# Kernel tuning notes

Measured on AMD Instinct MI355X. Metric: run time of the kernel, lower is better.

The kernel has to match this reference:

```python
import jax, jax.numpy as jnp
import numpy as np

GRID_SIZE = 3
LN_EPS = 1e-5
BASIS_EPS = 1e-6


def setup_inputs() -> dict:
    key = jax.random.key(0)
    ks = jax.random.split(key, 5)
    B, S, D_IN, D_OUT, SE_H = 8, 1024, 1024, 1024, 32
    x = jax.random.normal(ks[0], (B, S, D_IN), dtype=jnp.float32)
    base_weight = jax.random.normal(ks[1], (D_OUT, D_IN), dtype=jnp.float32) * 0.01
    spline_weight = jax.random.normal(ks[2], (D_OUT, D_IN, GRID_SIZE), dtype=jnp.float32) * 0.005
    ln_w = jnp.ones((D_OUT,), dtype=jnp.float32)
    ln_b = jnp.zeros((D_OUT,), dtype=jnp.float32)
    se_w1 = jax.random.normal(ks[3], (SE_H, D_OUT), dtype=jnp.float32) * 0.03
    se_b1 = jnp.zeros((SE_H,), dtype=jnp.float32)
    se_w2 = jax.random.normal(ks[4], (D_OUT, SE_H), dtype=jnp.float32) * 0.03
    se_b2 = jnp.zeros((D_OUT,), dtype=jnp.float32)
    return {"x": x, "base_weight": base_weight, "spline_weight": spline_weight,
            "ln_w": ln_w, "ln_b": ln_b, "se_w1": se_w1, "se_b1": se_b1,
            "se_w2": se_w2, "se_b2": se_b2}


def _kan_layer(x2d, base_weight, spline_weight, ln_w, ln_b, se_w1, se_b1, se_w2, se_b2):
    # x2d: [N, D_in]
    base = x2d @ base_weight.T                                   # [N, D_out]
    grid = jnp.linspace(-1.0, 1.0, GRID_SIZE).astype(x2d.dtype)  # [G]
    dist = jnp.abs(x2d[..., None] - grid)                        # [N, D_in, G]
    basis = jnp.where(dist < 1.0, (1.0 - dist) ** 2, 0.0)
    basis = basis / (basis.sum(axis=-1, keepdims=True) + BASIS_EPS)
    spline = jnp.einsum('nig,oig->no', basis, spline_weight)     # [N, D_out]
    out = base + spline
    # LayerNorm (dropout is identity at inference)
    mu = out.mean(axis=-1, keepdims=True)
    var = ((out - mu) ** 2).mean(axis=-1, keepdims=True)
    out = (out - mu) * jax.lax.rsqrt(var + LN_EPS) * ln_w + ln_b
    # SE gating (2D branch: applied per flattened token)
    h = jnp.maximum(out @ se_w1.T + se_b1, 0.0)
    se = jax.nn.sigmoid(h @ se_w2.T + se_b2)
    return out * se


def reference(x, base_weight, spline_weight, ln_w, ln_b, se_w1, se_b1, se_w2, se_b2):
    B, S, D = x.shape
    out = _kan_layer(x.reshape(-1, D), base_weight, spline_weight,
                     ln_w, ln_b, se_w1, se_b1, se_w2, se_b2)
    return out.reshape(B, S, -1)
```

## Files before the change

### kernel.cpp

```cpp
#include <hip/hip_runtime.h>
#include <hip/hip_bf16.h>
#include <math.h>

typedef __attribute__((ext_vector_type(8))) __bf16 bf16x8;
typedef __attribute__((ext_vector_type(4))) float f32x4;

#define NTOK 8192
#define DIN 1024
#define DOUT 1024
#define KAUG 4096
#define SEH 32

#define BK 64
#define NKT (KAUG / BK)

static __device__ __forceinline__ unsigned short f2bf(float f) {
  union { float f; unsigned u; } v; v.f = f;
  unsigned r = (v.u + 0x7FFFu + ((v.u >> 16) & 1u)) >> 16;
  return (unsigned short)r;
}

__global__ __launch_bounds__(256) void prep(const float* __restrict__ x,
                                            const float* __restrict__ bw,
                                            const float* __restrict__ sw,
                                            const float* __restrict__ w1,
                                            const float* __restrict__ w2,
                                            ushort* __restrict__ Aaug,
                                            ushort* __restrict__ Waug,
                                            ushort* __restrict__ w1b,
                                            ushort* __restrict__ w2b) {
  const int b = blockIdx.x;
  if (b < 32768) {
    const int id = b * 256 + threadIdx.x;
    const float v = x[id];
    const float d0 = fabsf(v + 1.f), d1 = fabsf(v), d2 = fabsf(v - 1.f);
    float b0 = (d0 < 1.f) ? (1.f - d0) * (1.f - d0) : 0.f;
    float b1 = (d1 < 1.f) ? (1.f - d1) * (1.f - d1) : 0.f;
    float b2 = (d2 < 1.f) ? (1.f - d2) * (1.f - d2) : 0.f;
    const float inv = 1.f / (b0 + b1 + b2 + 1e-6f);
    ushort4 o;
    o.x = f2bf(v);
    o.y = f2bf(b0 * inv);
    o.z = f2bf(b1 * inv);
    o.w = f2bf(b2 * inv);
    ((ushort4*)Aaug)[id] = o;
  } else if (b < 32768 + 4096) {
    const int id = (b - 32768) * 256 + threadIdx.x;
    ushort4 o;
    o.x = f2bf(bw[id]);
    o.y = f2bf(sw[id * 3 + 0]);
    o.z = f2bf(sw[id * 3 + 1]);
    o.w = f2bf(sw[id * 3 + 2]);
    ((ushort4*)Waug)[id] = o;
  } else {
    const int id = (b - 32768 - 4096) * 256 + threadIdx.x;
    if (id < SEH * DOUT) w1b[id] = f2bf(w1[id]);
    else w2b[id - SEH * DOUT] = f2bf(w2[id - SEH * DOUT]);
  }
}

#define WAITVM(N) asm volatile("s_waitcnt vmcnt(" #N ")" ::: "memory")

__global__ __launch_bounds__(256, 2) void gemm_ns(const ushort* __restrict__ A,
                                                  const ushort* __restrict__ B,
                                                  float* __restrict__ C) {
  __shared__ ushort As[2][128 * BK];
  __shared__ ushort Bs[2][128 * BK];
  const int tid = threadIdx.x;
  const int wid = tid >> 6, lane = tid & 63;
  const int l16 = lane & 15, lk = lane >> 4;
  const int wm = wid >> 1, wn = wid & 1;

  const int g = (blockIdx.x & 7) * 64 + (blockIdx.x >> 3);
  const int bm = g >> 3;
  const int bn = g & 7;

  const ushort* Ab = A + (size_t)bm * 128 * KAUG;
  const ushort* Bb = B + (size_t)bn * 128 * KAUG;

  const int lrow = lane >> 3;
  const int lcb = (lane & 7) ^ lrow;

  const int aBase = (wm * 64 + l16) * 64;
  const int bBase = (wn * 64 + l16) * 64;
  const int sw0 = ((l16 & 4) << 3) + ((lk ^ (l16 & 3)) << 3);
  const int sw1 = sw0 ^ 32;

  f32x4 acc[4][4] = {};

#define STAGE_A(kt, buf, r)                                                     \
  __builtin_amdgcn_global_load_lds(                                             \
      (const __attribute__((address_space(1))) void*)(Ab +                      \
          (size_t)((r) * 32 + wid * 8 + lrow) * KAUG + (kt) * BK + lcb * 8),    \
      (__attribute__((address_space(3))) void*)(&As[buf][((r) * 256 + wid * 64) * 8]), \
      16, 0, 0)
#define STAGE_B(kt, buf, r)                                                     \
  __builtin_amdgcn_global_load_lds(                                             \
      (const __attribute__((address_space(1))) void*)(Bb +                      \
          (size_t)((r) * 32 + wid * 8 + lrow) * KAUG + (kt) * BK + lcb * 8),    \
      (__attribute__((address_space(3))) void*)(&Bs[buf][((r) * 256 + wid * 64) * 8]), \
      16, 0, 0)
#define STAGE_ALL(kt, buf)                                                      \
  do {                                                                          \
    STAGE_A(kt, buf, 0); STAGE_A(kt, buf, 1); STAGE_A(kt, buf, 2); STAGE_A(kt, buf, 3); \
    STAGE_B(kt, buf, 0); STAGE_B(kt, buf, 1); STAGE_B(kt, buf, 2); STAGE_B(kt, buf, 3); \
  } while (0)

#define TILE(kt, CB, NB)                                                        \
  do {                                                                          \
    if ((kt) < NKT - 1) {                                                       \
      STAGE_ALL((kt) + 1, NB);                                                  \
      WAITVM(8);                                                                \
    } else {                                                                    \
      WAITVM(0);                                                                \
    }                                                                           \
    __builtin_amdgcn_s_barrier();                                               \
    bf16x8 af0[4], bf0[4], af1[4], bf1[4];                                      \
    _Pragma("unroll")                                                           \
    for (int m = 0; m < 4; ++m) af0[m] = *(const bf16x8*)&As[CB][aBase + m * 1024 + sw0]; \
    _Pragma("unroll")                                                           \
    for (int n = 0; n < 4; ++n) bf0[n] = *(const bf16x8*)&Bs[CB][bBase + n * 1024 + sw0]; \
    __builtin_amdgcn_s_setprio(1);                                              \
    _Pragma("unroll")                                                           \
    for (int m = 0; m < 4; ++m)                                                 \
      _Pragma("unroll")                                                         \
      for (int n = 0; n < 4; ++n)                                               \
        acc[m][n] = __builtin_amdgcn_mfma_f32_16x16x32_bf16(                    \
            af0[m], bf0[n], acc[m][n], 0, 0, 0);                                \
    __builtin_amdgcn_s_setprio(0);                                              \
    _Pragma("unroll")                                                           \
    for (int m = 0; m < 4; ++m) af1[m] = *(const bf16x8*)&As[CB][aBase + m * 1024 + sw1]; \
    _Pragma("unroll")                                                           \
    for (int n = 0; n < 4; ++n) bf1[n] = *(const bf16x8*)&Bs[CB][bBase + n * 1024 + sw1]; \
    __builtin_amdgcn_s_setprio(1);                                              \
    _Pragma("unroll")                                                           \
    for (int m = 0; m < 4; ++m)                                                 \
      _Pragma("unroll")                                                         \
      for (int n = 0; n < 4; ++n)                                               \
        acc[m][n] = __builtin_amdgcn_mfma_f32_16x16x32_bf16(                    \
            af1[m], bf1[n], acc[m][n], 0, 0, 0);                                \
    __builtin_amdgcn_s_setprio(0);                                              \
    __builtin_amdgcn_s_barrier();                                               \
  } while (0)

  STAGE_ALL(0, 0);

  for (int kt2 = 0; kt2 < NKT; kt2 += 2) {
    TILE(kt2, 0, 1);
    TILE(kt2 + 1, 1, 0);
  }

  float* Cb = C + (size_t)(bm * 128 + wm * 64) * DOUT + bn * 128 + wn * 64;
#pragma unroll
  for (int m = 0; m < 4; ++m)
#pragma unroll
    for (int n = 0; n < 4; ++n)
#pragma unroll
      for (int j = 0; j < 4; ++j)
        Cb[(size_t)(m * 16 + lk * 4 + j) * DOUT + n * 16 + l16] = acc[m][n][j];
}

__global__ __launch_bounds__(256) void ln_se_mfma(
    float* __restrict__ out,
    const float* __restrict__ ln_w, const float* __restrict__ ln_b,
    const ushort* __restrict__ w1b, const float* __restrict__ se_b1,
    const ushort* __restrict__ w2b, const float* __restrict__ se_b2) {
  __shared__ float Yl[16 * 1028];
  __shared__ float Hpart[4][512];
  __shared__ unsigned Hb[256];
  const int tid = threadIdx.x;
  const int w = tid >> 6, lane = tid & 63;
  const int l16 = lane & 15, lk = lane >> 4;
  const int tok0 = blockIdx.x * 16;

  float4 lwv[4], lbv[4];
#pragma unroll
  for (int q = 0; q < 4; ++q) {
    lwv[q] = ((const float4*)ln_w)[q * 64 + lane];
    lbv[q] = ((const float4*)ln_b)[q * 64 + lane];
  }

  for (int qt = 0; qt < 4; ++qt) {
    const int tl = w * 4 + qt;
    const float4* r0 = (const float4*)(out + (size_t)(tok0 + tl) * DOUT);
    float4 v[4];
#pragma unroll
    for (int q = 0; q < 4; ++q) v[q] = r0[q * 64 + lane];
    float s = 0.f, ss = 0.f;
#pragma unroll
    for (int q = 0; q < 4; ++q) {
      s += v[q].x + v[q].y + v[q].z + v[q].w;
      ss += v[q].x * v[q].x + v[q].y * v[q].y + v[q].z * v[q].z + v[q].w * v[q].w;
    }
#pragma unroll
    for (int m = 32; m; m >>= 1) { s += __shfl_xor(s, m); ss += __shfl_xor(ss, m); }
    const float mu = s * (1.f / (float)DOUT);
    const float inv = rsqrtf(ss * (1.f / (float)DOUT) - mu * mu + 1e-5f);
#pragma unroll
    for (int q = 0; q < 4; ++q) {
      float4 yv;
      yv.x = (v[q].x - mu) * inv * lwv[q].x + lbv[q].x;
      yv.y = (v[q].y - mu) * inv * lwv[q].y + lbv[q].y;
      yv.z = (v[q].z - mu) * inv * lwv[q].z + lbv[q].z;
      yv.w = (v[q].w - mu) * inv * lwv[q].w + lbv[q].w;
      *(float4*)&Yl[tl * 1028 + (q * 64 + lane) * 4] = yv;
    }
  }
  __syncthreads();

  f32x4 acc1[2] = {};
#pragma unroll
  for (int s = 0; s < 8; ++s) {
    const int ks = w * 8 + s;
    const int k = ks * 32 + lk * 8;
    const float* yp = &Yl[l16 * 1028 + k];
    const f32x4 q0 = *(const f32x4*)yp;
    const f32x4 q1 = *(const f32x4*)(yp + 4);
    bf16x8 af;
    af[0] = (__bf16)q0[0]; af[1] = (__bf16)q0[1];
    af[2] = (__bf16)q0[2]; af[3] = (__bf16)q0[3];
    af[4] = (__bf16)q1[0]; af[5] = (__bf16)q1[1];
    af[6] = (__bf16)q1[2]; af[7] = (__bf16)q1[3];
#pragma unroll
    for (int nt = 0; nt < 2; ++nt) {
      const bf16x8 bf = *(const bf16x8*)(w1b + (nt * 16 + l16) * 1024 + ks * 32 + lk * 8);
      acc1[nt] = __builtin_amdgcn_mfma_f32_16x16x32_bf16(af, bf, acc1[nt], 0, 0, 0);
    }
  }
#pragma unroll
  for (int nt = 0; nt < 2; ++nt)
#pragma unroll
    for (int j = 0; j < 4; ++j)
      Hpart[w][(lk * 4 + j) * 32 + nt * 16 + l16] = acc1[nt][j];
  __syncthreads();

  {
    const int e2 = tid * 2;
    float h0 = Hpart[0][e2] + Hpart[1][e2] + Hpart[2][e2] + Hpart[3][e2];
    float h1 = Hpart[0][e2 + 1] + Hpart[1][e2 + 1] + Hpart[2][e2 + 1] + Hpart[3][e2 + 1];
    h0 = fmaxf(h0 + se_b1[e2 & 31], 0.f);
    h1 = fmaxf(h1 + se_b1[(e2 & 31) + 1], 0.f);
    Hb[tid] = (unsigned)f2bf(h0) | ((unsigned)f2bf(h1) << 16);
  }
  __syncthreads();

  union { uint4 u; bf16x8 v; } ha;
  ha.u = *(const uint4*)&Hb[l16 * 16 + lk * 4];
  const int nbase = w * 256;
#pragma unroll
  for (int nt = 0; nt < 16; ++nt) {
    const int col = nbase + nt * 16 + l16;
    const bf16x8 bf = *(const bf16x8*)(w2b + col * 32 + lk * 8);
    f32x4 gz = {0.f, 0.f, 0.f, 0.f};
    gz = __builtin_amdgcn_mfma_f32_16x16x32_bf16(ha.v, bf, gz, 0, 0, 0);
    const float b2 = se_b2[col];
#pragma unroll
    for (int j = 0; j < 4; ++j) {
      const int tl = lk * 4 + j;
      const float sg = 1.f / (1.f + __expf(-(gz[j] + b2)));
      out[(size_t)(tok0 + tl) * DOUT + col] = Yl[tl * 1028 + col] * sg;
    }
  }
}

extern "C" void kernel_launch(void* const* d_in, const int* in_sizes, int n_in,
                              void* d_out, int out_size, void* d_ws, size_t ws_size,
                              hipStream_t stream) {
  const float* x = (const float*)d_in[0];
  const float* bw = (const float*)d_in[1];
  const float* sw = (const float*)d_in[2];
  const float* ln_w = (const float*)d_in[3];
  const float* ln_b = (const float*)d_in[4];
  const float* se_w1 = (const float*)d_in[5];
  const float* se_b1 = (const float*)d_in[6];
  const float* se_w2 = (const float*)d_in[7];
  const float* se_b2 = (const float*)d_in[8];
  float* out = (float*)d_out;

  ushort* Aaug = (ushort*)d_ws;
  ushort* Waug = Aaug + (size_t)NTOK * KAUG;
  ushort* w1b = Waug + (size_t)DOUT * KAUG;
  ushort* w2b = w1b + SEH * DOUT;

  prep<<<32768 + 4096 + 256, 256, 0, stream>>>(x, bw, sw, se_w1, se_w2,
                                               Aaug, Waug, w1b, w2b);
  gemm_ns<<<512, 256, 0, stream>>>(Aaug, Waug, out);
  ln_se_mfma<<<NTOK / 16, 256, 0, stream>>>(out, ln_w, ln_b,
                                            w1b, se_b1, w2b, se_b2);
}
```

Before: 107.9 us.

## Switch GEMM to 256x128 tiles, 8 waves, triple-buffered LDS pipeline

Replaces the 128x128 double-buffered GEMM with a 256x128 tile run by 512 threads (8 waves), using a three-stage LDS ring. Prefetches two tiles ahead, splitting each tile's global-to-LDS loads into two halves interleaved with the two MFMA phases, and uses sched barriers plus explicit lgkmcnt waits. The goal is better load/compute overlap and more reuse of B per block. In exchange it uses more LDS per block (3×(256+128)×64 bf16 = 144KB), which may limit occupancy to one block per CU despite launch_bounds(512,2), and it adds more barriers per K-step.

Result: slower. 154.2 us (+42.9%).

```diff
diff --git a/kernel.cpp b/kernel.cpp
--- a/kernel.cpp
+++ b/kernel.cpp
@@ -11,6 +11,8 @@
 #define KAUG 4096
 #define SEH 32
 
+#define BM 256
+#define BN 128
 #define BK 64
 #define NKT (KAUG / BK)
 
@@ -60,26 +62,28 @@
 }
 
 #define WAITVM(N) asm volatile("s_waitcnt vmcnt(" #N ")" ::: "memory")
-
-__global__ __launch_bounds__(256, 2) void gemm_ns(const ushort* __restrict__ A,
-                                                  const ushort* __restrict__ B,
-                                                  float* __restrict__ C) {
-  __shared__ ushort As[2][128 * BK];
-  __shared__ ushort Bs[2][128 * BK];
+#define LGKM0() asm volatile("s_waitcnt lgkmcnt(0)" ::: "memory")
+#define SB0() __builtin_amdgcn_sched_barrier(0)
+
+__global__ __launch_bounds__(512, 2) void gemm8p(const ushort* __restrict__ A,
+                                                 const ushort* __restrict__ B,
+                                                 float* __restrict__ C) {
+  __shared__ ushort As[3][BM * BK];
+  __shared__ ushort Bs[3][BN * BK];
   const int tid = threadIdx.x;
   const int wid = tid >> 6, lane = tid & 63;
   const int l16 = lane & 15, lk = lane >> 4;
   const int wm = wid >> 1, wn = wid & 1;
 
-  const int g = (blockIdx.x & 7) * 64 + (blockIdx.x >> 3);
+  const int g = (blockIdx.x & 7) * 32 + (blockIdx.x >> 3);
   const int bm = g >> 3;
   const int bn = g & 7;
 
-  const ushort* Ab = A + (size_t)bm * 128 * KAUG;
-  const ushort* Bb = B + (size_t)bn * 128 * KAUG;
-
-  const int lrow = lane >> 3;
-  const int lcb = (lane & 7) ^ lrow;
+  const ushort* Ab = A + (size_t)bm * BM * KAUG;
+  const ushort* Bb = B + (size_t)bn * BN * KAUG;
+
+  const int srow = tid >> 3;
+  const int scol = (tid & 7) ^ (srow & 7);
 
   const int aBase = (wm * 64 + l16) * 64;
   const int bBase = (wn * 64 + l16) * 64;
@@ -91,66 +95,77 @@
 #define STAGE_A(kt, buf, r)                                                     \
   __builtin_amdgcn_global_load_lds(                                             \
       (const __attribute__((address_space(1))) void*)(Ab +                      \
-          (size_t)((r) * 32 + wid * 8 + lrow) * KAUG + (kt) * BK + lcb * 8),    \
-      (__attribute__((address_space(3))) void*)(&As[buf][((r) * 256 + wid * 64) * 8]), \
+          (size_t)((r) * 64 + srow) * KAUG + (kt) * BK + scol * 8),             \
+      (__attribute__((address_space(3))) void*)(&As[buf][((r) * 512 + tid) * 8]), \
       16, 0, 0)
 #define STAGE_B(kt, buf, r)                                                     \
   __builtin_amdgcn_global_load_lds(                                             \
       (const __attribute__((address_space(1))) void*)(Bb +                      \
-          (size_t)((r) * 32 + wid * 8 + lrow) * KAUG + (kt) * BK + lcb * 8),    \
-      (__attribute__((address_space(3))) void*)(&Bs[buf][((r) * 256 + wid * 64) * 8]), \
+          (size_t)((r) * 64 + srow) * KAUG + (kt) * BK + scol * 8),             \
+      (__attribute__((address_space(3))) void*)(&Bs[buf][((r) * 512 + tid) * 8]), \
       16, 0, 0)
-#define STAGE_ALL(kt, buf)                                                      \
+#define STAGE6(kt, buf)                                                         \
   do {                                                                          \
-    STAGE_A(kt, buf, 0); STAGE_A(kt, buf, 1); STAGE_A(kt, buf, 2); STAGE_A(kt, buf, 3); \
-    STAGE_B(kt, buf, 0); STAGE_B(kt, buf, 1); STAGE_B(kt, buf, 2); STAGE_B(kt, buf, 3); \
+    STAGE_A(kt, buf, 0); STAGE_A(kt, buf, 1); STAGE_A(kt, buf, 2);              \
+    STAGE_A(kt, buf, 3); STAGE_B(kt, buf, 0); STAGE_B(kt, buf, 1);              \
   } while (0)
 
-#define TILE(kt, CB, NB)                                                        \
-  do {                                                                          \
-    if ((kt) < NKT - 1) {                                                       \
-      STAGE_ALL((kt) + 1, NB);                                                  \
-      WAITVM(8);                                                                \
-    } else {                                                                    \
-      WAITVM(0);                                                                \
-    }                                                                           \
-    __builtin_amdgcn_s_barrier();                                               \
-    bf16x8 af0[4], bf0[4], af1[4], bf1[4];                                      \
-    _Pragma("unroll")                                                           \
-    for (int m = 0; m < 4; ++m) af0[m] = *(const bf16x8*)&As[CB][aBase + m * 1024 + sw0]; \
-    _Pragma("unroll")                                                           \
-    for (int n = 0; n < 4; ++n) bf0[n] = *(const bf16x8*)&Bs[CB][bBase + n * 1024 + sw0]; \
-    __builtin_amdgcn_s_setprio(1);                                              \
-    _Pragma("unroll")                                                           \
-    for (int m = 0; m < 4; ++m)                                                 \
-      _Pragma("unroll")                                                         \
-      for (int n = 0; n < 4; ++n)                                               \
-        acc[m][n] = __builtin_amdgcn_mfma_f32_16x16x32_bf16(                    \
-            af0[m], bf0[n], acc[m][n], 0, 0, 0);                                \
-    __builtin_amdgcn_s_setprio(0);                                              \
-    _Pragma("unroll")                                                           \
-    for (int m = 0; m < 4; ++m) af1[m] = *(const bf16x8*)&As[CB][aBase + m * 1024 + sw1]; \
-    _Pragma("unroll")                                                           \
-    for (int n = 0; n < 4; ++n) bf1[n] = *(const bf16x8*)&Bs[CB][bBase + n * 1024 + sw1]; \
-    __builtin_amdgcn_s_setprio(1);                                              \
-    _Pragma("unroll")                                                           \
-    for (int m = 0; m < 4; ++m)                                                 \
-      _Pragma("unroll")                                                         \
-      for (int n = 0; n < 4; ++n)                                               \
-        acc[m][n] = __builtin_amdgcn_mfma_f32_16x16x32_bf16(                    \
-            af1[m], bf1[n], acc[m][n], 0, 0, 0);                                \
-    __builtin_amdgcn_s_setprio(0);                                              \
-    __builtin_amdgcn_s_barrier();                                               \
-  } while (0)
-
-  STAGE_ALL(0, 0);
-
-  for (int kt2 = 0; kt2 < NKT; kt2 += 2) {
-    TILE(kt2, 0, 1);
-    TILE(kt2 + 1, 1, 0);
-  }
-
-  float* Cb = C + (size_t)(bm * 128 + wm * 64) * DOUT + bn * 128 + wn * 64;
+  STAGE6(0, 0);
+  STAGE6(1, 1);
+  WAITVM(6);
+  __builtin_amdgcn_s_barrier();
+  SB0();
+
+  int c = 0;
+  for (int kt = 0; kt < NKT; ++kt) {
+    int s = c + 2; if (s >= 3) s -= 3;
+    const ushort* Ac = As[c];
+    const ushort* Bc = Bs[c];
+    const bool pf = (kt < NKT - 2);
+
+    if (pf) { STAGE_A(kt + 2, s, 0); STAGE_A(kt + 2, s, 1); STAGE_B(kt + 2, s, 0); }
+    bf16x8 af0[4], bf0[4];
+#pragma unroll
+    for (int m = 0; m < 4; ++m) af0[m] = *(const bf16x8*)&Ac[aBase + m * 1024 + sw0];
+#pragma unroll
+    for (int n = 0; n < 4; ++n) bf0[n] = *(const bf16x8*)&Bc[bBase + n * 1024 + sw0];
+    __builtin_amdgcn_s_barrier();
+    LGKM0();
+    SB0();
+    __builtin_amdgcn_s_setprio(1);
+#pragma unroll
+    for (int m = 0; m < 4; ++m)
+#pragma unroll
+      for (int n = 0; n < 4; ++n)
+        acc[m][n] = __builtin_amdgcn_mfma_f32_16x16x32_bf16(af0[m], bf0[n], acc[m][n], 0, 0, 0);
+    __builtin_amdgcn_s_setprio(0);
+    __builtin_amdgcn_s_barrier();
+    SB0();
+
+    if (pf) { STAGE_A(kt + 2, s, 2); STAGE_A(kt + 2, s, 3); STAGE_B(kt + 2, s, 1); }
+    bf16x8 af1[4], bf1[4];
+#pragma unroll
+    for (int m = 0; m < 4; ++m) af1[m] = *(const bf16x8*)&Ac[aBase + m * 1024 + sw1];
+#pragma unroll
+    for (int n = 0; n < 4; ++n) bf1[n] = *(const bf16x8*)&Bc[bBase + n * 1024 + sw1];
+    if (pf) { WAITVM(6); } else if (kt == NKT - 2) { WAITVM(0); }
+    __builtin_amdgcn_s_barrier();
+    LGKM0();
+    SB0();
+    __builtin_amdgcn_s_setprio(1);
+#pragma unroll
+    for (int m = 0; m < 4; ++m)
+#pragma unroll
+      for (int n = 0; n < 4; ++n)
+        acc[m][n] = __builtin_amdgcn_mfma_f32_16x16x32_bf16(af1[m], bf1[n], acc[m][n], 0, 0, 0);
+    __builtin_amdgcn_s_setprio(0);
+    __builtin_amdgcn_s_barrier();
+    SB0();
+
+    c += 1; if (c == 3) c = 0;
+  }
+
+  float* Cb = C + (size_t)(bm * BM + wm * 64) * DOUT + bn * BN + wn * 64;
 #pragma unroll
   for (int m = 0; m < 4; ++m)
 #pragma unroll
@@ -284,7 +299,7 @@
 
   prep<<<32768 + 4096 + 256, 256, 0, stream>>>(x, bw, sw, se_w1, se_w2,
                                                Aaug, Waug, w1b, w2b);
-  gemm_ns<<<512, 256, 0, stream>>>(Aaug, Waug, out);
+  gemm8p<<<(NTOK / BM) * (DOUT / BN), 512, 0, stream>>>(Aaug, Waug, out);
   ln_se_mfma<<<NTOK / 16, 256, 0, stream>>>(out, ln_w, ln_b,
                                             w1b, se_b1, w2b, se_b2);
 }
```
